# Optimization experiments

Hardware: AMD Instinct MI355X
Metric: run time of the kernel (lower is better)

## Reference

```python
import jax, jax.numpy as jnp
import numpy as np

VOCAB_SIZE = 119547  # bert-base-multilingual-cased
B, S, H = 64, 512, 768


def setup_inputs() -> dict:
    key = jax.random.key(0)
    k1, k2, k3, k4 = jax.random.split(key, 4)
    hidden_states = jax.random.normal(k1, (B, S, H), dtype=jnp.float32)
    input_ids = jax.random.randint(k2, (B, S), 0, VOCAB_SIZE, dtype=jnp.int64)
    attention_mask = jnp.ones((B, S), dtype=jnp.int32)
    W1 = jax.random.normal(k3, (H, H), dtype=jnp.float32) * (1.0 / np.sqrt(H))
    b1 = jnp.zeros((H,), dtype=jnp.float32)
    W2 = jax.random.normal(k4, (H, 1), dtype=jnp.float32) * (1.0 / np.sqrt(H))
    b2 = jnp.zeros((1,), dtype=jnp.float32)
    return {"hidden_states": hidden_states, "input_ids": input_ids,
            "attention_mask": attention_mask, "W1": W1, "b1": b1, "W2": W2, "b2": b2}


def reference(hidden_states, input_ids, attention_mask, W1, b1, W2, b2):
    # token_importance MLP (dropout = identity at eval): [B,S,H] -> [B,S]
    h = jax.nn.relu(jnp.einsum('bsh,hk->bsk', hidden_states, W1) + b1)
    importance = (jnp.einsum('bsh,ho->bso', h, W2) + b2)[..., 0]  # [B,S]
    token_weights = jnp.log1p(jax.nn.relu(importance)) * attention_mask.astype(jnp.float32)
    # scatter-max into vocab-sized sparse doc vector.
    # Masked positions have weight 0; buffer init 0 and weights >= 0, so
    # scattering 0 is equivalent to skipping them (matches the torch loop).
    batch_idx = jnp.arange(hidden_states.shape[0])[:, None]  # [B,1]
    sparse_repr = jnp.zeros((hidden_states.shape[0], VOCAB_SIZE), dtype=token_weights.dtype)
    sparse_repr = sparse_repr.at[batch_idx, input_ids].max(token_weights)
    return sparse_repr, token_weights
```

## Files before the change

kernel.cpp:

```cpp
#include <hip/hip_runtime.h>
#include <math.h>
#include <stdint.h>

#define VOCAB 119547
#define NB    64
#define NS    512
#define NH    768
#define M_TOT (NB * NS)

typedef _Float16 half8_t __attribute__((ext_vector_type(8)));
typedef _Float16 half4_t __attribute__((ext_vector_type(4)));
typedef float f32x4 __attribute__((ext_vector_type(4)));

#define WAITVM(N) asm volatile("s_waitcnt vmcnt(" #N ")" ::: "memory")
#define WAITLGKM() asm volatile("s_waitcnt lgkmcnt(0)" ::: "memory")
#define SCHEDB() __builtin_amdgcn_sched_barrier(0)

__device__ __forceinline__ void gload_lds16(const void* g, void* l) {
    __builtin_amdgcn_global_load_lds(
        (const __attribute__((address_space(1))) uint32_t*)g,
        (__attribute__((address_space(3))) uint32_t*)l, 16, 0, 0);
}

__global__ void prep_w1t(const float* __restrict__ W1, _Float16* __restrict__ W1T) {
    long i = (long)blockIdx.x * blockDim.x + threadIdx.x;
    if (i >= (long)NH * NH / 4) return;
    int n  = (int)(i / (NH / 4));
    int k4 = (int)(i % (NH / 4)) * 4;
    half4_t h;
#pragma unroll
    for (int q = 0; q < 4; ++q) h[q] = (_Float16)W1[(long)(k4 + q) * NH + n];
    ((half4_t*)W1T)[i] = h;
}

__global__ __launch_bounds__(256, 4) void gemm_f16(
    const float* __restrict__ X,
    const _Float16* __restrict__ W1T,
    const float* __restrict__ b1,
    const float* __restrict__ W2v,
    float* __restrict__ imp)
{
    __shared__ __align__(16) _Float16 As[2][128 * 32];
    __shared__ __align__(16) _Float16 Bs[2][128 * 32];

    const int tid  = threadIdx.x;
    const int lane = tid & 63;
    const int wid  = tid >> 6;
    const int wm   = wid >> 1;
    const int wn   = wid & 1;

    const int bid = blockIdx.x;
    const int wg  = (bid & 7) * 192 + (bid >> 3);
    const int nt  = wg % 6;
    const int mt  = wg / 6;
    const int m0  = mt * 128;
    const int n0  = nt * 128;

    const int c0 = tid, c1 = tid + 256;
    const int r0 = c0 >> 2, r1 = c1 >> 2;
    const int sk0 = ((c0 & 3) ^ ((r0 >> 1) & 3)) * 8;
    const int sk1 = ((c1 & 3) ^ ((r1 >> 1) & 3)) * 8;
    const _Float16* gB0 = W1T + (long)(n0 + r0) * NH + sk0;
    const _Float16* gB1 = W1T + (long)(n0 + r1) * NH + sk1;

    const int ar = tid >> 3;
    const int kc = tid & 7;
    const float* gA = X + (long)(m0 + ar) * NH + kc * 4;
    const int aw = ((kc >> 1) ^ ((ar >> 1) & 3)) * 8 + (kc & 1) * 4;

    const int lr = lane & 15;
    const int ls = lane >> 4;
    const int s2 = ls ^ ((lr >> 1) & 3);
    int offA[4], offB[4];
#pragma unroll
    for (int f = 0; f < 4; ++f) {
        offA[f] = (wm * 64 + f * 16 + lr) * 32 + s2 * 8;
        offB[f] = (wn * 64 + f * 16 + lr) * 32 + s2 * 8;
    }

    f32x4 acc[4][4];
#pragma unroll
    for (int a = 0; a < 4; ++a)
#pragma unroll
        for (int b = 0; b < 4; ++b) acc[a][b] = (f32x4){0.f, 0.f, 0.f, 0.f};

    float4 ArA[4], ArB[4];

#define LOADA(T, AR)                                                        \
    _Pragma("unroll") for (int i = 0; i < 4; ++i)                           \
        AR[i] = *(const float4*)(gA + (T) * 32 + (long)i * 32 * NH);

#define CVTWRITE(BUF, AR)                                                   \
    _Pragma("unroll") for (int i = 0; i < 4; ++i) {                         \
        half4_t h;                                                          \
        h[0] = (_Float16)AR[i].x; h[1] = (_Float16)AR[i].y;                 \
        h[2] = (_Float16)AR[i].z; h[3] = (_Float16)AR[i].w;                 \
        *(half4_t*)(As[BUF] + (ar + 32 * i) * 32 + aw) = h;                 \
    }

#define STAGEB(T, BUF)                                                      \
    gload_lds16(gB0 + (T) * 32, Bs[BUF] + c0 * 8);                          \
    gload_lds16(gB1 + (T) * 32, Bs[BUF] + c1 * 8);

#define COMPUTE(BUF)                                                        \
    {                                                                       \
        half8_t af[4], bf[4];                                               \
        _Pragma("unroll") for (int f = 0; f < 4; ++f)                       \
            af[f] = *(const half8_t*)(As[BUF] + offA[f]);                   \
        _Pragma("unroll") for (int f = 0; f < 4; ++f)                       \
            bf[f] = *(const half8_t*)(Bs[BUF] + offB[f]);                   \
        _Pragma("unroll") for (int a = 0; a < 4; ++a)                       \
            _Pragma("unroll") for (int b = 0; b < 4; ++b)                   \
                acc[a][b] = __builtin_amdgcn_mfma_f32_16x16x32_f16(         \
                    af[a], bf[b], acc[a][b], 0, 0, 0);                      \
    }

#define KSTEP(T, CUR, NXT, ARC, ARL)                                        \
    STAGEB((T) + 1, NXT);                                                   \
    SCHEDB();                                                               \
    LOADA(((T) + 2 > 23 ? 23 : (T) + 2), ARL);                              \
    COMPUTE(CUR);                                                           \
    WAITVM(6);                                                              \
    CVTWRITE(NXT, ARC);                                                     \
    WAITVM(4);                                                              \
    WAITLGKM();                                                             \
    __builtin_amdgcn_s_barrier();                                           \
    SCHEDB();

    LOADA(0, ArA);
    SCHEDB();
    STAGEB(0, 0);
    WAITVM(2);
    CVTWRITE(0, ArA);
    LOADA(1, ArA);
    WAITVM(4);
    WAITLGKM();
    __builtin_amdgcn_s_barrier();
    SCHEDB();

#pragma unroll 1
    for (int t = 0; t < 22; t += 2) {
        KSTEP(t, 0, 1, ArA, ArB);
        KSTEP(t + 1, 1, 0, ArB, ArA);
    }
    KSTEP(22, 0, 1, ArA, ArB);
    COMPUTE(1);

#undef LOADA
#undef CVTWRITE
#undef STAGEB
#undef COMPUTE
#undef KSTEP

    float b1v[4], w2v[4];
#pragma unroll
    for (int f = 0; f < 4; ++f) {
        int col = n0 + wn * 64 + f * 16 + lr;
        b1v[f] = b1[col];
        w2v[f] = W2v[col];
    }
#pragma unroll
    for (int a = 0; a < 4; ++a)
#pragma unroll
        for (int reg = 0; reg < 4; ++reg) {
            float p = 0.f;
#pragma unroll
            for (int f = 0; f < 4; ++f) {
                float h = fmaxf(acc[a][f][reg] + b1v[f], 0.f);
                p = fmaf(h, w2v[f], p);
            }
            p += __shfl_xor(p, 1);
            p += __shfl_xor(p, 2);
            p += __shfl_xor(p, 4);
            p += __shfl_xor(p, 8);
            if (lr == 0) {
                int row = m0 + wm * 64 + a * 16 + ls * 4 + reg;
                atomicAdd(&imp[row], p);
            }
        }
}

__global__ void finalize(const float* __restrict__ imp,
                         const float* __restrict__ b2,
                         const int* __restrict__ mask,
                         const int* __restrict__ ids,
                         float* __restrict__ tw_out,
                         float* __restrict__ sparse) {
    int i = blockIdx.x * blockDim.x + threadIdx.x;
    if (i >= M_TOT) return;
    float v = fmaxf(imp[i] + b2[0], 0.f);
    float tw = log1pf(v) * (float)mask[i];
    tw_out[i] = tw;
    int b  = i >> 9;
    int id = ids[i];
    unsigned int* addr = (unsigned int*)&sparse[(long)b * VOCAB + id];
    atomicMax(addr, __float_as_uint(tw));
}

__global__ __launch_bounds__(256) void gemm_importance(
    const float* __restrict__ X, const float* __restrict__ W1,
    const float* __restrict__ b1, const float* __restrict__ W2v,
    float* __restrict__ imp)
{
    __shared__ float As_[16][64];
    __shared__ float Bs_[16][128];
    const int tid = threadIdx.x;
    const int m0 = blockIdx.x * 64, n0 = blockIdx.y * 128;
    const int tx = tid & 31, ty = tid >> 5;
    float acc[8][4];
#pragma unroll
    for (int r = 0; r < 8; ++r)
#pragma unroll
        for (int c = 0; c < 4; ++c) acc[r][c] = 0.f;
    const int arow = tid >> 2, ac = (tid & 3) * 4;
    const float* Xp = X + (long)(m0 + arow) * NH + ac;
    for (int k0 = 0; k0 < NH; k0 += 16) {
        float4 av = *(const float4*)(Xp + k0);
        As_[ac + 0][arow] = av.x; As_[ac + 1][arow] = av.y;
        As_[ac + 2][arow] = av.z; As_[ac + 3][arow] = av.w;
        int f = tid, br = f >> 5, bc = (f & 31) * 4;
        *(float4*)&Bs_[br][bc] = *(const float4*)&W1[(long)(k0 + br) * NH + n0 + bc];
        f = tid + 256; br = f >> 5; bc = (f & 31) * 4;
        *(float4*)&Bs_[br][bc] = *(const float4*)&W1[(long)(k0 + br) * NH + n0 + bc];
        __syncthreads();
#pragma unroll
        for (int k = 0; k < 16; ++k) {
            float4 a0 = *(const float4*)&As_[k][ty * 8];
            float4 a1 = *(const float4*)&As_[k][ty * 8 + 4];
            float4 bv = *(const float4*)&Bs_[k][tx * 4];
            float a[8] = {a0.x, a0.y, a0.z, a0.w, a1.x, a1.y, a1.z, a1.w};
            float bb[4] = {bv.x, bv.y, bv.z, bv.w};
#pragma unroll
            for (int r = 0; r < 8; ++r)
#pragma unroll
                for (int c = 0; c < 4; ++c)
                    acc[r][c] = fmaf(a[r], bb[c], acc[r][c]);
        }
        __syncthreads();
    }
    float b1v[4], w2v[4];
#pragma unroll
    for (int c = 0; c < 4; ++c) {
        int col = n0 + tx * 4 + c;
        b1v[c] = b1[col]; w2v[c] = W2v[col];
    }
#pragma unroll
    for (int r = 0; r < 8; ++r) {
        float p = 0.f;
#pragma unroll
        for (int c = 0; c < 4; ++c)
            p = fmaf(fmaxf(acc[r][c] + b1v[c], 0.f), w2v[c], p);
#pragma unroll
        for (int mdel = 16; mdel >= 1; mdel >>= 1) p += __shfl_xor(p, mdel);
        if (tx == 0) atomicAdd(&imp[m0 + ty * 8 + r], p);
    }
}

extern "C" void kernel_launch(void* const* d_in, const int* in_sizes, int n_in,
                              void* d_out, int out_size, void* d_ws, size_t ws_size,
                              hipStream_t stream) {
    const float* X    = (const float*)d_in[0];
    const int*   ids  = (const int*)d_in[1];
    const int*   mask = (const int*)d_in[2];
    const float* W1   = (const float*)d_in[3];
    const float* b1   = (const float*)d_in[4];
    const float* W2   = (const float*)d_in[5];
    const float* b2   = (const float*)d_in[6];

    float* sparse = (float*)d_out;
    float* tw_out = sparse + (long)NB * VOCAB;
    float* imp    = (float*)d_ws;

    const size_t impB = (size_t)M_TOT * 4;
    const size_t W1TB = (size_t)NH * NH * 2;

    hipMemsetAsync(sparse, 0, (size_t)NB * VOCAB * 4, stream);
    hipMemsetAsync(imp, 0, impB, stream);

    if (ws_size >= impB + W1TB) {
        _Float16* W1T = (_Float16*)((char*)d_ws + impB);
        prep_w1t<<<(NH * NH / 4 + 255) / 256, 256, 0, stream>>>(W1, W1T);
        gemm_f16<<<(M_TOT / 128) * (NH / 128), 256, 0, stream>>>(
            X, W1T, b1, W2, imp);
    } else {
        dim3 grid(M_TOT / 64, NH / 128);
        gemm_importance<<<grid, 256, 0, stream>>>(X, W1, b1, W2, imp);
    }
    finalize<<<M_TOT / 256, 256, 0, stream>>>(imp, b2, mask, ids, tw_out, sparse);
}
```

Baseline: 266.0 us.

## Pre-convert X to fp16 and use triple-buffered async LDS loads for both operands

Adds a prep pass that converts the whole activation matrix X to fp16 in workspace, alongside the W1 transpose. The GEMM then loads both A and B straight into LDS with global_load_lds, through a three-stage buffer ring, instead of reading fp32 A into registers and converting it in the loop. This drops register staging and conversion work from the inner loop and deepens the prefetch. The cost is an extra full read of X (about 100 MB fp32) and a 50 MB fp16 write plus re-read, more LDS per block, and lower launch-bounds occupancy (3 instead of 4).

Result: faster. 240.4 us (-9.6%).

```diff
diff --git a/kernel.cpp b/kernel.cpp
--- a/kernel.cpp
+++ b/kernel.cpp
@@ -22,26 +22,43 @@
         (__attribute__((address_space(3))) uint32_t*)l, 16, 0, 0);
 }
 
-__global__ void prep_w1t(const float* __restrict__ W1, _Float16* __restrict__ W1T) {
+__global__ void prep(const float* __restrict__ X, const float* __restrict__ W1,
+                     _Float16* __restrict__ Xh, _Float16* __restrict__ W1T) {
     long i = (long)blockIdx.x * blockDim.x + threadIdx.x;
-    if (i >= (long)NH * NH / 4) return;
-    int n  = (int)(i / (NH / 4));
-    int k4 = (int)(i % (NH / 4)) * 4;
-    half4_t h;
-#pragma unroll
-    for (int q = 0; q < 4; ++q) h[q] = (_Float16)W1[(long)(k4 + q) * NH + n];
-    ((half4_t*)W1T)[i] = h;
-}
-
-__global__ __launch_bounds__(256, 4) void gemm_f16(
-    const float* __restrict__ X,
+    long stride = (long)gridDim.x * blockDim.x;
+    const long nx8 = (long)M_TOT * NH / 8;
+    const float4* X4 = (const float4*)X;
+    half8_t* Xh8 = (half8_t*)Xh;
+    for (long j = i; j < nx8; j += stride) {
+        float4 a = X4[2 * j], b = X4[2 * j + 1];
+        half8_t h;
+        h[0] = (_Float16)a.x; h[1] = (_Float16)a.y;
+        h[2] = (_Float16)a.z; h[3] = (_Float16)a.w;
+        h[4] = (_Float16)b.x; h[5] = (_Float16)b.y;
+        h[6] = (_Float16)b.z; h[7] = (_Float16)b.w;
+        Xh8[j] = h;
+    }
+    const long nw8 = (long)NH * NH / 8;
+    half8_t* W1T8 = (half8_t*)W1T;
+    for (long j = i; j < nw8; j += stride) {
+        int n  = (int)(j / (NH / 8));
+        int k8 = (int)(j % (NH / 8)) * 8;
+        half8_t h;
+#pragma unroll
+        for (int q = 0; q < 8; ++q) h[q] = (_Float16)W1[(long)(k8 + q) * NH + n];
+        W1T8[j] = h;
+    }
+}
+
+__global__ __launch_bounds__(256, 3) void gemm_f16(
+    const _Float16* __restrict__ Xh,
     const _Float16* __restrict__ W1T,
     const float* __restrict__ b1,
     const float* __restrict__ W2v,
     float* __restrict__ imp)
 {
-    __shared__ __align__(16) _Float16 As[2][128 * 32];
-    __shared__ __align__(16) _Float16 Bs[2][128 * 32];
+    __shared__ __align__(16) _Float16 As[3][128 * 32];
+    __shared__ __align__(16) _Float16 Bs[3][128 * 32];
 
     const int tid  = threadIdx.x;
     const int lane = tid & 63;
@@ -60,13 +77,10 @@
     const int r0 = c0 >> 2, r1 = c1 >> 2;
     const int sk0 = ((c0 & 3) ^ ((r0 >> 1) & 3)) * 8;
     const int sk1 = ((c1 & 3) ^ ((r1 >> 1) & 3)) * 8;
+    const _Float16* gA0 = Xh  + (long)(m0 + r0) * NH + sk0;
+    const _Float16* gA1 = Xh  + (long)(m0 + r1) * NH + sk1;
     const _Float16* gB0 = W1T + (long)(n0 + r0) * NH + sk0;
     const _Float16* gB1 = W1T + (long)(n0 + r1) * NH + sk1;
-
-    const int ar = tid >> 3;
-    const int kc = tid & 7;
-    const float* gA = X + (long)(m0 + ar) * NH + kc * 4;
-    const int aw = ((kc >> 1) ^ ((ar >> 1) & 3)) * 8 + (kc & 1) * 4;
 
     const int lr = lane & 15;
     const int ls = lane >> 4;
@@ -84,21 +98,9 @@
 #pragma unroll
         for (int b = 0; b < 4; ++b) acc[a][b] = (f32x4){0.f, 0.f, 0.f, 0.f};
 
-    float4 ArA[4], ArB[4];
-
-#define LOADA(T, AR)                                                        \
-    _Pragma("unroll") for (int i = 0; i < 4; ++i)                           \
-        AR[i] = *(const float4*)(gA + (T) * 32 + (long)i * 32 * NH);
-
-#define CVTWRITE(BUF, AR)                                                   \
-    _Pragma("unroll") for (int i = 0; i < 4; ++i) {                         \
-        half4_t h;                                                          \
-        h[0] = (_Float16)AR[i].x; h[1] = (_Float16)AR[i].y;                 \
-        h[2] = (_Float16)AR[i].z; h[3] = (_Float16)AR[i].w;                 \
-        *(half4_t*)(As[BUF] + (ar + 32 * i) * 32 + aw) = h;                 \
-    }
-
-#define STAGEB(T, BUF)                                                      \
+#define STAGE(T, BUF)                                                       \
+    gload_lds16(gA0 + (T) * 32, As[BUF] + c0 * 8);                          \
+    gload_lds16(gA1 + (T) * 32, As[BUF] + c1 * 8);                          \
     gload_lds16(gB0 + (T) * 32, Bs[BUF] + c0 * 8);                          \
     gload_lds16(gB1 + (T) * 32, Bs[BUF] + c1 * 8);
 
@@ -115,40 +117,38 @@
                     af[a], bf[b], acc[a][b], 0, 0, 0);                      \
     }
 
-#define KSTEP(T, CUR, NXT, ARC, ARL)                                        \
-    STAGEB((T) + 1, NXT);                                                   \
+#define KSTEP(TSTG, CURB, STGB)                                             \
+    STAGE(TSTG, STGB);                                                      \
     SCHEDB();                                                               \
-    LOADA(((T) + 2 > 23 ? 23 : (T) + 2), ARL);                              \
-    COMPUTE(CUR);                                                           \
-    WAITVM(6);                                                              \
-    CVTWRITE(NXT, ARC);                                                     \
+    COMPUTE(CURB);                                                          \
     WAITVM(4);                                                              \
     WAITLGKM();                                                             \
     __builtin_amdgcn_s_barrier();                                           \
     SCHEDB();
 
-    LOADA(0, ArA);
-    SCHEDB();
-    STAGEB(0, 0);
-    WAITVM(2);
-    CVTWRITE(0, ArA);
-    LOADA(1, ArA);
+    STAGE(0, 0);
+    STAGE(1, 1);
     WAITVM(4);
     WAITLGKM();
     __builtin_amdgcn_s_barrier();
     SCHEDB();
 
 #pragma unroll 1
-    for (int t = 0; t < 22; t += 2) {
-        KSTEP(t, 0, 1, ArA, ArB);
-        KSTEP(t + 1, 1, 0, ArB, ArA);
-    }
-    KSTEP(22, 0, 1, ArA, ArB);
+    for (int tt = 0; tt < 7; ++tt) {
+        const int t3 = 3 * tt;
+        KSTEP(t3 + 2, 0, 2);
+        KSTEP(t3 + 3, 1, 0);
+        KSTEP(t3 + 4, 2, 1);
+    }
+    KSTEP(23, 0, 2);
     COMPUTE(1);
-
-#undef LOADA
-#undef CVTWRITE
-#undef STAGEB
+    WAITVM(0);
+    WAITLGKM();
+    __builtin_amdgcn_s_barrier();
+    SCHEDB();
+    COMPUTE(2);
+
+#undef STAGE
 #undef COMPUTE
 #undef KSTEP
 
@@ -272,16 +272,18 @@
     float* imp    = (float*)d_ws;
 
     const size_t impB = (size_t)M_TOT * 4;
+    const size_t XhB  = (size_t)M_TOT * NH * 2;
     const size_t W1TB = (size_t)NH * NH * 2;
 
     hipMemsetAsync(sparse, 0, (size_t)NB * VOCAB * 4, stream);
     hipMemsetAsync(imp, 0, impB, stream);
 
-    if (ws_size >= impB + W1TB) {
-        _Float16* W1T = (_Float16*)((char*)d_ws + impB);
-        prep_w1t<<<(NH * NH / 4 + 255) / 256, 256, 0, stream>>>(W1, W1T);
+    if (ws_size >= impB + XhB + W1TB) {
+        _Float16* Xh  = (_Float16*)((char*)d_ws + impB);
+        _Float16* W1T = (_Float16*)((char*)d_ws + impB + XhB);
+        prep<<<2048, 256, 0, stream>>>(X, W1, Xh, W1T);
         gemm_f16<<<(M_TOT / 128) * (NH / 128), 256, 0, stream>>>(
-            X, W1T, b1, W2, imp);
+            Xh, W1T, b1, W2, imp);
     } else {
         dim3 grid(M_TOT / 64, NH / 128);
         gemm_importance<<<grid, 256, 0, stream>>>(X, W1, b1, W2, imp);
```
